# Optimization experiments

Measured on AMD Instinct MI355X. Metric: run time of the kernel, lower is better.

The kernel has to match this reference:

```python
import jax, jax.numpy as jnp
import numpy as np

B, N_IN, D, K, N = 8, 256, 128, 1024, 4096
EMA_GAMMA = 0.99


def setup_inputs() -> dict:
    key = jax.random.key(0)
    k1, k2, k3 = jax.random.split(key, 3)
    z = jax.random.normal(k1, (B, N_IN, N), dtype=jnp.float32)
    # Conv1d(n_in, d, 1, bias=False) == a (d, n_in) matmul; xavier-ish scale
    W_lin = jax.random.normal(k2, (D, N_IN), dtype=jnp.float32) * (1.0 / np.sqrt(N_IN))
    # codebook initialized xavier_uniform with gain=10 in the original
    lim = 10.0 * np.sqrt(6.0 / (K + D))
    emb = jax.random.uniform(k3, (K, D), dtype=jnp.float32, minval=-lim, maxval=lim)
    ema_numer = emb * (1.0 - EMA_GAMMA)
    ema_denom = jnp.ones((K,), dtype=jnp.float32) * (1.0 - EMA_GAMMA)
    return {"z": z, "W_lin": W_lin, "emb": emb,
            "ema_numer": ema_numer, "ema_denom": ema_denom}


def reference(z, W_lin, emb, ema_numer, ema_denom):
    # ze: (B, d, N) -- 1x1 conv == channel matmul
    ze = jnp.einsum('bcn,dc->bdn', z, W_lin)
    sg_emb = jax.lax.stop_gradient(emb)           # codebook is stop-gradded

    # scaled L2 distance:  ||ze - q|| / (||ze|| + ||q||), shape (B, K, N)
    ze_sq = jnp.sum(ze * ze, axis=1)              # (B, N)
    q_sq = jnp.sum(sg_emb * sg_emb, axis=1)       # (K,)
    dots = jnp.einsum('bdn,kd->bkn', ze, sg_emb)  # (B, K, N)
    dist_sq = jnp.maximum(ze_sq[:, None, :] + q_sq[None, :, None] - 2.0 * dots, 0.0)
    den = jnp.sqrt(ze_sq)[:, None, :] + jnp.sqrt(q_sq)[None, :, None]
    snorm = jnp.sqrt(dist_sq) / den               # (B, K, N)

    min_ind = jnp.argmin(snorm, axis=1)           # (B, N) int
    zq = jnp.moveaxis(sg_emb[min_ind], -1, 1)     # (B, d, N)

    # ReplaceGrad: forward value = zq, gradient routed to ze (straight-through)
    zq_rg = ze + jax.lax.stop_gradient(zq - ze)

    # EMA codebook statistics (scatter-add over codebook indices)
    flat_ind = min_ind.reshape(-1)                             # (B*N,)
    ze_flat = jax.lax.stop_gradient(
        jnp.moveaxis(ze, 1, 2).reshape(-1, ze.shape[1]))       # (B*N, d)
    z_sum = jax.ops.segment_sum(ze_flat, flat_ind, num_segments=K)   # (K, d)
    n_sum = jax.ops.segment_sum(jnp.ones(flat_ind.shape, ze.dtype),
                                flat_ind, num_segments=K)            # (K,)
    ema_numer_new = EMA_GAMMA * ema_numer + (1.0 - EMA_GAMMA) * z_sum
    ema_denom_new = EMA_GAMMA * ema_denom + (1.0 - EMA_GAMMA) * n_sum
    return zq_rg, ema_numer_new, ema_denom_new
```

## Files before the change

kernel.cpp:

```cpp
#include <hip/hip_runtime.h>
#include <cmath>
#include <stdint.h>

#define B_    8
#define NIN_  256
#define D_    128
#define K_    1024
#define N_    4096
#define P_    (B_ * N_)
#define MARGIN_M 1e-4f

typedef __attribute__((ext_vector_type(8))) short bf16x8;
typedef __attribute__((ext_vector_type(4))) float f32x4;

#define WS_ZSUM   0
#define WS_CNT    524288
#define WS_FLAGC  528384
#define WS_MEMSET 532480
#define WS_OFF    532480
#define WS_QSQ    536576
#define WS_QNORM  540672
#define WS_KSTAR  544768
#define WS_RANK   675840
#define WS_PLIST  806912
#define WS_KLIST  937984
#define WS_FLIST  1069056
#define WS_WT     1200128
#define WS_ZPM    1331200
#define WS_ZESQ   18108416
#define WS_ZEN    18239488
#define WS_ZE2F   18370560
#define WS_EMB2F  43536384
#define WS_VAL1   44322816
#define WS_IDX1   46419968
#define WS_VAL2   48517120

__device__ inline unsigned short f2bf(float v) {
  union { float f; uint32_t u; } c; c.f = v;
  return (unsigned short)((c.u + 0x7FFFu + ((c.u >> 16) & 1u)) >> 16);
}
__device__ inline float bf2f(unsigned short b) {
  union { float f; uint32_t u; } c; c.u = ((uint32_t)b) << 16; return c.f;
}
__device__ inline uint32_t pack2(float a, float b, int lo) {
  unsigned short ha = f2bf(a); if (lo) ha = f2bf(a - bf2f(ha));
  unsigned short hb = f2bf(b); if (lo) hb = f2bf(b - bf2f(hb));
  return (uint32_t)ha | ((uint32_t)hb << 16);
}

__global__ __launch_bounds__(256) void prep_kernel(
    const float* __restrict__ W, const float* __restrict__ emb,
    float* __restrict__ Wt, float* __restrict__ q_sq, float* __restrict__ q_norm,
    uint4* __restrict__ emb2f)
{
  const int tid = threadIdx.x;
  const int bid = blockIdx.x;
  if (bid < 128) {
    int t = bid * 256 + tid;
    int c = t >> 7, d = t & 127;
    Wt[t] = W[d * NIN_ + c];
  } else if (bid < 132) {
    int k = (bid - 128) * 256 + tid;
    const float* e = emb + (size_t)k * D_;
    float s = 0.f;
    #pragma unroll 8
    for (int d = 0; d < D_; ++d) s = fmaf(e[d], e[d], s);
    q_sq[k] = s;
    q_norm[k] = sqrtf(s);
  } else {
    const int kt = bid - 132;
    #pragma unroll
    for (int i = 0; i < 3; ++i) {
      int f    = i * 256 + tid;
      int c    = f >> 6;
      int lane = f & 63;
      int k    = kt * 16 + (lane & 15);
      int q    = lane >> 4;
      int kk0  = c * 32 + q * 8;
      int lo   = (kk0 >> 7) == 1;
      int d0   = kk0 & 127;
      float4 v0 = *(const float4*)&emb[(size_t)k * D_ + d0];
      float4 v1 = *(const float4*)&emb[(size_t)k * D_ + d0 + 4];
      uint4 u;
      u.x = pack2(v0.x, v0.y, lo);
      u.y = pack2(v0.z, v0.w, lo);
      u.z = pack2(v1.x, v1.y, lo);
      u.w = pack2(v1.z, v1.w, lo);
      emb2f[(size_t)kt * 768 + f] = u;
    }
  }
}

__global__ __launch_bounds__(512) void ze_kernel(
    const float* __restrict__ z, const float* __restrict__ Wt,
    float* __restrict__ ze_pm, float* __restrict__ ze_sq,
    float* __restrict__ ze_norm, uint4* __restrict__ ze2f)
{
  __shared__ float tile[64][132];
  __shared__ float sqpart[8][64];
  const int t    = threadIdx.x;
  const int lane = t & 63;
  const int wv   = __builtin_amdgcn_readfirstlane(t >> 6);
  const int p    = blockIdx.x * 64 + lane;
  const int b    = p >> 12;
  const int n    = p & (N_ - 1);

  float acc[16];
  #pragma unroll
  for (int j = 0; j < 16; ++j) acc[j] = 0.f;
  const float* zp = z + (size_t)b * NIN_ * N_ + n;
  const float* wp = Wt + wv * 16;
  #pragma unroll 4
  for (int c = 0; c < NIN_; ++c) {
    float zv = zp[(size_t)c * N_];
    #pragma unroll
    for (int j = 0; j < 16; ++j)
      acc[j] = fmaf(wp[c * D_ + j], zv, acc[j]);
  }
  #pragma unroll
  for (int j = 0; j < 16; ++j) tile[lane][wv * 16 + j] = acc[j];
  float s = 0.f;
  #pragma unroll
  for (int j = 0; j < 16; ++j) s = fmaf(acc[j], acc[j], s);
  sqpart[wv][lane] = s;
  __syncthreads();
  if (wv == 0) {
    float tt = sqpart[0][lane];
    #pragma unroll
    for (int w = 1; w < 8; ++w) tt += sqpart[w][lane];
    ze_sq[p] = tt;
    ze_norm[p] = sqrtf(tt);
  }
  const int row = t >> 5;
  const int c4  = (t & 31) * 4;
  #pragma unroll
  for (int r = 0; r < 4; ++r) {
    int pr = r * 16 + row;
    float4 v = *(const float4*)&tile[pr][c4];
    *(float4*)&ze_pm[(size_t)(blockIdx.x * 64 + pr) * D_ + c4] = v;
  }
  #pragma unroll
  for (int i = 0; i < 6; ++i) {
    int f    = i * 512 + t;
    int lane_f = f & 63;
    int g    = f >> 6;
    int c    = g % 12;
    int lpt  = g / 12;
    int pl   = lpt * 16 + (lane_f & 15);
    int q    = lane_f >> 4;
    int kk0  = c * 32 + q * 8;
    int lo   = (kk0 >> 7) == 2;
    int d0   = kk0 & 127;
    float4 v0 = *(const float4*)&tile[pl][d0];
    float4 v1 = *(const float4*)&tile[pl][d0 + 4];
    uint4 u;
    u.x = pack2(v0.x, v0.y, lo);
    u.y = pack2(v0.z, v0.w, lo);
    u.z = pack2(v1.x, v1.y, lo);
    u.w = pack2(v1.z, v1.w, lo);
    ze2f[((size_t)(blockIdx.x * 4 + lpt) * 12 + c) * 64 + lane_f] = u;
  }
}

__global__ __launch_bounds__(512, 2) void mfma_argmin_kernel(
    const uint4* __restrict__ ze2f, const uint4* __restrict__ emb2f,
    const float* __restrict__ ze_sq, const float* __restrict__ ze_norm,
    const float* __restrict__ q_sq, const float* __restrict__ q_norm,
    float* __restrict__ val1, int* __restrict__ idx1, float* __restrict__ val2)
{
  __shared__ uint4 As[2][512];
  __shared__ uint4 Bs[2][1024];
  const int tid  = threadIdx.x;
  const int lane = tid & 63;
  const int tw   = tid >> 6;
  const int kb   = blockIdx.x & 3;
  const int pb   = blockIdx.x >> 2;
  const int wm   = tw & 1;
  const int wn   = tw >> 1;

  const uint4* a_base  = ze2f + ((size_t)(pb * 8 + tw) * 12) * 64 + lane;
  const uint4* b_base0 = emb2f + ((size_t)(kb * 16 + tw) * 12) * 64 + lane;
  const uint4* b_base1 = emb2f + ((size_t)(kb * 16 + tw + 8) * 12) * 64 + lane;

  f32x4 acc[4][4];
  #pragma unroll
  for (int i = 0; i < 4; ++i)
    #pragma unroll
    for (int j = 0; j < 4; ++j) acc[i][j] = (f32x4){0.f, 0.f, 0.f, 0.f};

  uint4 pa = a_base[0], pb0 = b_base0[0], pb1 = b_base1[0];
  for (int c = 0; c < 12; ++c) {
    const int buf = c & 1;
    As[buf][tid] = pa;
    Bs[buf][tid] = pb0;
    Bs[buf][512 + tid] = pb1;
    __syncthreads();
    if (c + 1 < 12) {
      pa  = a_base[(c + 1) * 64];
      pb0 = b_base0[(c + 1) * 64];
      pb1 = b_base1[(c + 1) * 64];
    }
    uint4 afr[4], bfr[4];
    #pragma unroll
    for (int i = 0; i < 4; ++i) afr[i] = As[buf][(wm * 4 + i) * 64 + lane];
    #pragma unroll
    for (int j = 0; j < 4; ++j) bfr[j] = Bs[buf][(wn * 4 + j) * 64 + lane];
    #pragma unroll
    for (int i = 0; i < 4; ++i) {
      union { uint4 u; bf16x8 h; } au; au.u = afr[i];
      #pragma unroll
      for (int j = 0; j < 4; ++j) {
        union { uint4 u; bf16x8 h; } bu; bu.u = bfr[j];
        acc[i][j] = __builtin_amdgcn_mfma_f32_16x16x32_bf16(au.h, bu.h,
                                                            acc[i][j], 0, 0, 0);
      }
    }
  }

  const int col = lane & 15;
  const int q   = lane >> 4;
  float qsq_l[4], qn_l[4]; int kg[4];
  #pragma unroll
  for (int j = 0; j < 4; ++j) {
    kg[j]    = kb * 256 + wn * 64 + j * 16 + col;
    qsq_l[j] = q_sq[kg[j]];
    qn_l[j]  = q_norm[kg[j]];
  }
  const int g = kb * 4 + wn;
  #pragma unroll
  for (int i = 0; i < 4; ++i) {
    const int pbase = pb * 128 + wm * 64 + i * 16 + q * 4;
    f32x4 zs = *(const f32x4*)&ze_sq[pbase];
    f32x4 zn = *(const f32x4*)&ze_norm[pbase];
    float m1r[4], m2r[4]; int k1r[4];
    #pragma unroll
    for (int r = 0; r < 4; ++r) { m1r[r] = 1e30f; m2r[r] = 1e30f; k1r[r] = 0; }
    #pragma unroll
    for (int j = 0; j < 4; ++j) {
      #pragma unroll
      for (int r = 0; r < 4; ++r) {
        float dsq = fmaxf(zs[r] + qsq_l[j] - 2.0f * acc[i][j][r], 0.0f);
        float den = zn[r] + qn_l[j];
        float rd  = __builtin_amdgcn_rcpf(den);
        float m   = dsq * rd * rd;
        bool take = m < m1r[r];
        float loser = take ? m1r[r] : m;
        if (take) { m1r[r] = m; k1r[r] = kg[j]; }
        m2r[r] = fminf(m2r[r], loser);
      }
    }
    #pragma unroll
    for (int ms = 1; ms <= 8; ms <<= 1) {
      #pragma unroll
      for (int r = 0; r < 4; ++r) {
        float om1 = __shfl_xor(m1r[r], ms);
        int   ok1 = __shfl_xor(k1r[r], ms);
        float om2 = __shfl_xor(m2r[r], ms);
        bool take = (om1 < m1r[r]) || (om1 == m1r[r] && ok1 < k1r[r]);
        float loser = take ? m1r[r] : om1;
        if (take) { m1r[r] = om1; k1r[r] = ok1; }
        m2r[r] = fminf(fminf(m2r[r], om2), loser);
      }
    }
    if (col == 0) {
      const size_t o = (size_t)g * P_ + pbase;
      *(float4*)&val1[o] = make_float4(m1r[0], m1r[1], m1r[2], m1r[3]);
      *(int4*)&idx1[o]   = make_int4(k1r[0], k1r[1], k1r[2], k1r[3]);
      *(float4*)&val2[o] = make_float4(m2r[0], m2r[1], m2r[2], m2r[3]);
    }
  }
}

__global__ __launch_bounds__(256) void resolve_kernel(
    const float* __restrict__ val1, const int* __restrict__ idx1,
    const float* __restrict__ val2, int* __restrict__ kstar,
    int* __restrict__ rank, int* __restrict__ counts,
    int* __restrict__ flaglist, int* __restrict__ flagcnt)
{
  const int p = blockIdx.x * 256 + threadIdx.x;
  float m1 = 1e30f, m2 = 1e30f; int k1 = 0;
  #pragma unroll
  for (int g = 0; g < 16; ++g) {
    float v1 = val1[(size_t)g * P_ + p];
    int   i1 = idx1[(size_t)g * P_ + p];
    float v2 = val2[(size_t)g * P_ + p];
    bool take = v1 < m1;
    float loser = take ? m1 : v1;
    if (take) { m1 = v1; k1 = i1; }
    m2 = fminf(fminf(m2, v2), loser);
  }
  kstar[p] = k1;
  if (m2 - m1 <= MARGIN_M) {
    int s = atomicAdd(flagcnt, 1);
    flaglist[s] = p;
  } else {
    rank[p] = atomicAdd(&counts[k1], 1);
  }
}

__global__ __launch_bounds__(256) void fallback_kernel(
    const float* __restrict__ ze_pm, const float* __restrict__ emb,
    const float* __restrict__ ze_sq, const float* __restrict__ ze_norm,
    const float* __restrict__ q_sq, const float* __restrict__ q_norm,
    const int* __restrict__ flaglist, const int* __restrict__ flagcnt,
    int* __restrict__ kstar, int* __restrict__ rank, int* __restrict__ counts)
{
  __shared__ float zlds[128];
  __shared__ float wbs[4];
  __shared__ int   wbk[4];
  const int tid  = threadIdx.x;
  const int lane = tid & 63;
  const int w    = tid >> 6;
  const int cnt  = *flagcnt;
  for (int i = blockIdx.x; i < cnt; i += gridDim.x) {
    const int p = flaglist[i];
    __syncthreads();
    if (tid < 128) zlds[tid] = ze_pm[(size_t)p * D_ + tid];
    __syncthreads();
    const float zsq = ze_sq[p], zn = ze_norm[p];
    float bs = 1e30f; int bk = 0;
    #pragma unroll
    for (int tt = 0; tt < 4; ++tt) {
      const int k = (w * 4 + tt) * 64 + lane;
      const float* e = emb + (size_t)k * D_;
      float dot = 0.f;
      #pragma unroll 8
      for (int d = 0; d < D_; ++d)
        dot = fmaf(zlds[d], e[d], dot);
      float dsq = fmaxf(fmaf(-2.0f, dot, zsq + q_sq[k]), 0.0f);
      float sn  = sqrtf(dsq) / (zn + q_norm[k]);
      if (sn < bs) { bs = sn; bk = k; }
    }
    #pragma unroll
    for (int m = 1; m <= 32; m <<= 1) {
      float ov = __shfl_xor(bs, m);
      int   ok = __shfl_xor(bk, m);
      if (ov < bs || (ov == bs && ok < bk)) { bs = ov; bk = ok; }
    }
    if (lane == 0) { wbs[w] = bs; wbk[w] = bk; }
    __syncthreads();
    if (tid == 0) {
      float fb = wbs[0]; int fk = wbk[0];
      #pragma unroll
      for (int ww = 1; ww < 4; ++ww) {
        if (wbs[ww] < fb) { fb = wbs[ww]; fk = wbk[ww]; }
      }
      kstar[p] = fk;
      rank[p] = atomicAdd(&counts[fk], 1);
    }
  }
}

__global__ __launch_bounds__(1024) void prefix_kernel(
    const int* __restrict__ counts, const float* __restrict__ ema_denom,
    int* __restrict__ offsets, float* __restrict__ out_den)
{
  __shared__ int s[1024];
  const int t = threadIdx.x;
  const int c = counts[t];
  s[t] = c;
  __syncthreads();
  for (int off = 1; off < 1024; off <<= 1) {
    int v = (t >= off) ? s[t - off] : 0;
    __syncthreads();
    s[t] += v;
    __syncthreads();
  }
  offsets[t] = s[t] - c;
  out_den[t] = 0.99f * ema_denom[t] + 0.01f * (float)c;
}

__global__ __launch_bounds__(256) void scatter_kernel(
    const int* __restrict__ kstar, const int* __restrict__ rank,
    const int* __restrict__ offsets, int* __restrict__ pos_list,
    int* __restrict__ k_list)
{
  const int p = blockIdx.x * 256 + threadIdx.x;
  const int k = kstar[p];
  const int slot = offsets[k] + rank[p];
  pos_list[slot] = p;
  k_list[slot] = k;
}

__global__ __launch_bounds__(512) void zq_kernel(
    const float* __restrict__ ze_pm, const float* __restrict__ emb,
    const int* __restrict__ kstar, float* __restrict__ out)
{
  const int tid = threadIdx.x;
  const int lane = tid & 63;
  const int w = __builtin_amdgcn_readfirstlane(tid >> 6);
  const int p = blockIdx.x * 64 + lane;
  const int b = p >> 12;
  const int n = p & (N_ - 1);
  const int kst = kstar[p];
  const float* zr = ze_pm + (size_t)p * D_ + w * 16;
  const float* ek = emb + (size_t)kst * D_ + w * 16;
  float* op = out + (size_t)b * D_ * N_ + (size_t)(w * 16) * N_ + n;
  float4 zv[4], ev[4];
  #pragma unroll
  for (int r = 0; r < 4; ++r) {
    zv[r] = *(const float4*)&zr[r * 4];
    ev[r] = *(const float4*)&ek[r * 4];
  }
  #pragma unroll
  for (int r = 0; r < 4; ++r) {
    const float* zc = (const float*)&zv[r];
    const float* ec = (const float*)&ev[r];
    #pragma unroll
    for (int jj = 0; jj < 4; ++jj) {
      float zev = zc[jj];
      op[(size_t)(r * 4 + jj) * N_] = zev + (ec[jj] - zev);
    }
  }
}

__global__ __launch_bounds__(128) void gsum_kernel(
    const float* __restrict__ ze_pm, const int* __restrict__ pos_list,
    const int* __restrict__ k_list, float* __restrict__ z_sum)
{
  const int d  = threadIdx.x;
  const int i0 = blockIdx.x * 32;
  int   kprev = -1;
  float acc = 0.f;
  #pragma unroll
  for (int ii = 0; ii < 32; ++ii) {
    int p = pos_list[i0 + ii];
    int k = k_list[i0 + ii];
    if (k != kprev) {
      if (kprev >= 0) atomicAdd(&z_sum[(size_t)kprev * D_ + d], acc);
      acc = 0.f;
      kprev = k;
    }
    acc += ze_pm[(size_t)p * D_ + d];
  }
  if (kprev >= 0) atomicAdd(&z_sum[(size_t)kprev * D_ + d], acc);
}

__global__ __launch_bounds__(256) void finalize_num_kernel(
    const float* __restrict__ ema_numer, const float* __restrict__ z_sum,
    float* __restrict__ out)
{
  const int t = blockIdx.x * 256 + threadIdx.x;
  float* out_num = out + (size_t)B_ * D_ * N_;
  out_num[t] = 0.99f * ema_numer[t] + 0.01f * z_sum[t];
}

extern "C" void kernel_launch(void* const* d_in, const int* in_sizes, int n_in,
                              void* d_out, int out_size, void* d_ws, size_t ws_size,
                              hipStream_t stream)
{
  (void)in_sizes; (void)n_in; (void)out_size; (void)ws_size;
  const float* z         = (const float*)d_in[0];
  const float* W         = (const float*)d_in[1];
  const float* emb       = (const float*)d_in[2];
  const float* ema_numer = (const float*)d_in[3];
  const float* ema_denom = (const float*)d_in[4];
  float* out = (float*)d_out;
  char*  ws  = (char*)d_ws;
  float* z_sum   = (float*)(ws + WS_ZSUM);
  int*   counts  = (int*)(ws + WS_CNT);
  int*   flagcnt = (int*)(ws + WS_FLAGC);
  int*   offsets = (int*)(ws + WS_OFF);
  float* q_sq    = (float*)(ws + WS_QSQ);
  float* q_norm  = (float*)(ws + WS_QNORM);
  int*   kstar   = (int*)(ws + WS_KSTAR);
  int*   rank    = (int*)(ws + WS_RANK);
  int*   plist   = (int*)(ws + WS_PLIST);
  int*   klist   = (int*)(ws + WS_KLIST);
  int*   flist   = (int*)(ws + WS_FLIST);
  float* Wt      = (float*)(ws + WS_WT);
  float* ze_pm   = (float*)(ws + WS_ZPM);
  float* ze_sq   = (float*)(ws + WS_ZESQ);
  float* ze_norm = (float*)(ws + WS_ZEN);
  uint4* ze2f    = (uint4*)(ws + WS_ZE2F);
  uint4* emb2f   = (uint4*)(ws + WS_EMB2F);
  float* val1    = (float*)(ws + WS_VAL1);
  int*   idx1    = (int*)(ws + WS_IDX1);
  float* val2    = (float*)(ws + WS_VAL2);
  float* out_den = out + (size_t)B_ * D_ * N_ + K_ * D_;

  hipMemsetAsync(ws, 0, WS_MEMSET, stream);

  prep_kernel<<<196, 256, 0, stream>>>(W, emb, Wt, q_sq, q_norm, emb2f);
  ze_kernel<<<P_ / 64, 512, 0, stream>>>(z, Wt, ze_pm, ze_sq, ze_norm, ze2f);
  mfma_argmin_kernel<<<1024, 512, 0, stream>>>(ze2f, emb2f, ze_sq, ze_norm,
                                               q_sq, q_norm, val1, idx1, val2);
  resolve_kernel<<<P_ / 256, 256, 0, stream>>>(val1, idx1, val2, kstar,
                                               rank, counts, flist, flagcnt);
  fallback_kernel<<<1024, 256, 0, stream>>>(ze_pm, emb, ze_sq, ze_norm,
                                            q_sq, q_norm, flist, flagcnt,
                                            kstar, rank, counts);
  prefix_kernel<<<1, 1024, 0, stream>>>(counts, ema_denom, offsets, out_den);
  scatter_kernel<<<P_ / 256, 256, 0, stream>>>(kstar, rank, offsets, plist, klist);
  zq_kernel<<<P_ / 64, 512, 0, stream>>>(ze_pm, emb, kstar, out);
  gsum_kernel<<<P_ / 32, 128, 0, stream>>>(ze_pm, plist, klist, z_sum);
  finalize_num_kernel<<<K_ * D_ / 256, 256, 0, stream>>>(ema_numer, z_sum, out);
}
```

Baseline: 262.5 us.

## Load MFMA fragments directly from global memory, drop LDS staging and barriers

The argmin GEMM kernel stops staging A/B fragments through shared memory with a per-chunk __syncthreads. Each wave now loads its own 4 A and 4 B fragments straight from global memory into registers, double-buffered, with a fully unrolled chunk loop. The grid is remapped to 2048 blocks of 256 threads, with a swizzled block-to-tile mapping so that blocks sharing a point tile run near each other. This removes LDS traffic and barrier stalls, but loses the cross-wave sharing of loaded tiles and raises global/L2 load volume and register pressure.

After: 254.1 us. -3.2%, faster.

```diff
diff --git a/kernel.cpp b/kernel.cpp
--- a/kernel.cpp
+++ b/kernel.cpp
@@ -162,57 +162,54 @@
   }
 }
 
-__global__ __launch_bounds__(512, 2) void mfma_argmin_kernel(
+__global__ __launch_bounds__(256, 3) void mfma_argmin_kernel(
     const uint4* __restrict__ ze2f, const uint4* __restrict__ emb2f,
     const float* __restrict__ ze_sq, const float* __restrict__ ze_norm,
     const float* __restrict__ q_sq, const float* __restrict__ q_norm,
     float* __restrict__ val1, int* __restrict__ idx1, float* __restrict__ val2)
 {
-  __shared__ uint4 As[2][512];
-  __shared__ uint4 Bs[2][1024];
   const int tid  = threadIdx.x;
   const int lane = tid & 63;
-  const int tw   = tid >> 6;
-  const int kb   = blockIdx.x & 3;
-  const int pb   = blockIdx.x >> 2;
-  const int wm   = tw & 1;
-  const int wn   = tw >> 1;
-
-  const uint4* a_base  = ze2f + ((size_t)(pb * 8 + tw) * 12) * 64 + lane;
-  const uint4* b_base0 = emb2f + ((size_t)(kb * 16 + tw) * 12) * 64 + lane;
-  const uint4* b_base1 = emb2f + ((size_t)(kb * 16 + tw + 8) * 12) * 64 + lane;
+  const int w    = __builtin_amdgcn_readfirstlane(tid >> 6);
+  const int x    = blockIdx.x & 7;
+  const int ib   = blockIdx.x >> 3;
+  const int pb2  = x * 64 + (ib & 63);
+  const int kbb  = (ib >> 6) * 4 + w;
+
+  const uint4* a_base = ze2f  + (size_t)pb2 * 3072 + lane;
+  const uint4* b_base = emb2f + (size_t)kbb * 3072 + lane;
 
   f32x4 acc[4][4];
   #pragma unroll
-  for (int i = 0; i < 4; ++i)
-    #pragma unroll
-    for (int j = 0; j < 4; ++j) acc[i][j] = (f32x4){0.f, 0.f, 0.f, 0.f};
-
-  uint4 pa = a_base[0], pb0 = b_base0[0], pb1 = b_base1[0];
+  for (int ii = 0; ii < 4; ++ii)
+    #pragma unroll
+    for (int jj = 0; jj < 4; ++jj) acc[ii][jj] = (f32x4){0.f, 0.f, 0.f, 0.f};
+
+  uint4 af[2][4], bf[2][4];
+  #pragma unroll
+  for (int ii = 0; ii < 4; ++ii) af[0][ii] = a_base[ii * 768];
+  #pragma unroll
+  for (int jj = 0; jj < 4; ++jj) bf[0][jj] = b_base[jj * 768];
+
+  #pragma unroll
   for (int c = 0; c < 12; ++c) {
-    const int buf = c & 1;
-    As[buf][tid] = pa;
-    Bs[buf][tid] = pb0;
-    Bs[buf][512 + tid] = pb1;
-    __syncthreads();
+    const int cur = c & 1, nxt = cur ^ 1;
     if (c + 1 < 12) {
-      pa  = a_base[(c + 1) * 64];
-      pb0 = b_base0[(c + 1) * 64];
-      pb1 = b_base1[(c + 1) * 64];
-    }
-    uint4 afr[4], bfr[4];
-    #pragma unroll
-    for (int i = 0; i < 4; ++i) afr[i] = As[buf][(wm * 4 + i) * 64 + lane];
-    #pragma unroll
-    for (int j = 0; j < 4; ++j) bfr[j] = Bs[buf][(wn * 4 + j) * 64 + lane];
-    #pragma unroll
-    for (int i = 0; i < 4; ++i) {
-      union { uint4 u; bf16x8 h; } au; au.u = afr[i];
-      #pragma unroll
-      for (int j = 0; j < 4; ++j) {
-        union { uint4 u; bf16x8 h; } bu; bu.u = bfr[j];
-        acc[i][j] = __builtin_amdgcn_mfma_f32_16x16x32_bf16(au.h, bu.h,
-                                                            acc[i][j], 0, 0, 0);
+      #pragma unroll
+      for (int ii = 0; ii < 4; ++ii)
+        af[nxt][ii] = a_base[ii * 768 + (c + 1) * 64];
+      #pragma unroll
+      for (int jj = 0; jj < 4; ++jj)
+        bf[nxt][jj] = b_base[jj * 768 + (c + 1) * 64];
+    }
+    #pragma unroll
+    for (int ii = 0; ii < 4; ++ii) {
+      union { uint4 u; bf16x8 h; } au; au.u = af[cur][ii];
+      #pragma unroll
+      for (int jj = 0; jj < 4; ++jj) {
+        union { uint4 u; bf16x8 h; } bu; bu.u = bf[cur][jj];
+        acc[ii][jj] = __builtin_amdgcn_mfma_f32_16x16x32_bf16(au.h, bu.h,
+                                                              acc[ii][jj], 0, 0, 0);
       }
     }
   }
@@ -222,14 +219,14 @@
   float qsq_l[4], qn_l[4]; int kg[4];
   #pragma unroll
   for (int j = 0; j < 4; ++j) {
-    kg[j]    = kb * 256 + wn * 64 + j * 16 + col;
+    kg[j]    = kbb * 64 + j * 16 + col;
     qsq_l[j] = q_sq[kg[j]];
     qn_l[j]  = q_norm[kg[j]];
   }
-  const int g = kb * 4 + wn;
-  #pragma unroll
-  for (int i = 0; i < 4; ++i) {
-    const int pbase = pb * 128 + wm * 64 + i * 16 + q * 4;
+  const int g = kbb;
+  #pragma unroll
+  for (int ii = 0; ii < 4; ++ii) {
+    const int pbase = pb2 * 64 + ii * 16 + q * 4;
     f32x4 zs = *(const f32x4*)&ze_sq[pbase];
     f32x4 zn = *(const f32x4*)&ze_norm[pbase];
     float m1r[4], m2r[4]; int k1r[4];
@@ -239,7 +236,7 @@
     for (int j = 0; j < 4; ++j) {
       #pragma unroll
       for (int r = 0; r < 4; ++r) {
-        float dsq = fmaxf(zs[r] + qsq_l[j] - 2.0f * acc[i][j][r], 0.0f);
+        float dsq = fmaxf(zs[r] + qsq_l[j] - 2.0f * acc[ii][j][r], 0.0f);
         float den = zn[r] + qn_l[j];
         float rd  = __builtin_amdgcn_rcpf(den);
         float m   = dsq * rd * rd;
@@ -483,7 +480,7 @@
 
   prep_kernel<<<196, 256, 0, stream>>>(W, emb, Wt, q_sq, q_norm, emb2f);
   ze_kernel<<<P_ / 64, 512, 0, stream>>>(z, Wt, ze_pm, ze_sq, ze_norm, ze2f);
-  mfma_argmin_kernel<<<1024, 512, 0, stream>>>(ze2f, emb2f, ze_sq, ze_norm,
+  mfma_argmin_kernel<<<2048, 256, 0, stream>>>(ze2f, emb2f, ze_sq, ze_norm,
                                                q_sq, q_norm, val1, idx1, val2);
   resolve_kernel<<<P_ / 256, 256, 0, stream>>>(val1, idx1, val2, kstar,
                                                rank, counts, flist, flagcnt);
```
